# Kernel tuning notes

Measured on AMD Instinct MI355X. Metric: run time of the kernel, lower is better.

The kernel has to match this reference:

```python
import jax, jax.numpy as jnp
import numpy as np

N_QUBITS = 14
N_LAYERS = 6
BATCH = 512
DIM = 2 ** N_QUBITS

# Z expectation sign table: qubit 0 is the most-significant bit of the state index
_idx = np.arange(DIM)
_bits = np.stack([(_idx >> (N_QUBITS - 1 - q)) & 1 for q in range(N_QUBITS)])  # [n, DIM]
SIGNS = jnp.asarray(1.0 - 2.0 * _bits, dtype=jnp.float32)  # +1 for bit 0, -1 for bit 1


def _rx(theta):
    # 2x2 RX(theta) = [[cos(t/2), -i sin(t/2)], [-i sin(t/2), cos(t/2)]]
    c = jnp.cos(theta / 2).astype(jnp.complex64)
    s = ((-1j) * jnp.sin(theta / 2)).astype(jnp.complex64)
    return jnp.stack([jnp.stack([c, s]), jnp.stack([s, c])])


def _apply_1q(state, mat, q):
    # state: [B, 2^n] complex; apply 2x2 mat on qubit q
    left = 2 ** q
    right = 2 ** (N_QUBITS - 1 - q)
    s = state.reshape(-1, left, 2, right)
    s = jnp.einsum('ij,bljr->blir', mat, s)
    return s.reshape(-1, DIM)


def _apply_cnot(state, c, t):
    # CNOT(control=c, target=t): flip target bit where control bit is 1
    hi, lo = (c, t) if c < t else (t, c)
    A = 2 ** hi
    M = 2 ** (lo - hi - 1)
    R = 2 ** (N_QUBITS - 1 - lo)
    s = state.reshape(-1, A, 2, M, 2, R)
    if c < t:
        flipped = jnp.flip(s[:, :, 1:2, :, :, :], axis=4)
        s = jnp.concatenate([s[:, :, 0:1, :, :, :], flipped], axis=2)
    else:
        flipped = jnp.flip(s[:, :, :, :, 1:2, :], axis=2)
        s = jnp.concatenate([s[:, :, :, :, 0:1, :], flipped], axis=4)
    return s.reshape(-1, DIM)


def _forward(x, params):
    B = x.shape[0]
    # angle embedding in X basis: product state of RX(x_q)|0> per qubit
    half = 0.5 * x
    amps = jnp.stack([jnp.cos(half).astype(jnp.complex64),
                      ((-1j) * jnp.sin(half)).astype(jnp.complex64)], axis=-1)  # [B, n, 2]
    state = amps[:, 0]
    for q in range(1, N_QUBITS):
        state = (state[:, :, None] * amps[:, q][:, None, :]).reshape(B, -1)
    # basic_entangling ansatz: per-qubit RX then ring of CNOTs, per layer
    for layer in range(N_LAYERS):
        w = params[layer, 0]  # [n_qubits]
        for q in range(N_QUBITS):
            state = _apply_1q(state, _rx(w[q]), q)
        for q in range(N_QUBITS):
            state = _apply_cnot(state, q, (q + 1) % N_QUBITS)
    # <Z_q> expectation per qubit
    probs = state.real ** 2 + state.imag ** 2  # [B, DIM]
    return probs @ SIGNS.T  # [B, n_qubits]


def setup_inputs():
    key = jax.random.key(0)
    k1, k2 = jax.random.split(key)
    x = jax.random.normal(k1, (BATCH, N_QUBITS), dtype=jnp.float32)
    params = 2.0 * jnp.pi * jax.random.uniform(k2, (N_LAYERS, 1, N_QUBITS), dtype=jnp.float32)
    return {"x": x, "params": params}


def reference(x, params):
    return _forward(x, params)
```

## Files before the change

kernel.cpp:

```cpp
#include <hip/hip_runtime.h>
#include <math.h>


#define NQ 14
#define DIM 16384
#define NLAYERS 6
#define NGATES (NLAYERS * NQ)
#define BATCH 512
#define TB 1024
#define NREP 16
#define NSLICE 16
#define SLICE_B (BATCH / NSLICE)
#define B_PER_WAVE (SLICE_B * 64 / TB)

constexpr int cpopc(unsigned v) { int c = 0; while (v) { c += (int)(v & 1u); v >>= 1; } return c; }

constexpr unsigned cpext(unsigned v, unsigned m) {
    unsigned r = 0; int b = 0;
    for (int pos = 0; pos < 16; ++pos)
        if ((m >> pos) & 1u) { r |= ((v >> pos) & 1u) << b; ++b; }
    return r;
}

struct Tabs {
    unsigned short m[NGATES];
    unsigned short r[NQ];
    int p[NQ];
    int off[NQ + 1];
    unsigned char qb[NQ][NQ];
    int ng[NQ];
    unsigned short gmask[NQ][NGATES];
    unsigned char  gidx[NQ][NGATES];
};

constexpr Tabs gen_tabs() {
    Tabs T{};
    unsigned short C[NQ] = {}, R[NQ] = {};
    for (int q = 0; q < NQ; ++q) { C[q] = (unsigned short)(1u << (NQ - 1 - q)); R[q] = C[q]; }
    for (int l = 0; l < NLAYERS; ++l) {
        for (int q = 0; q < NQ; ++q) T.m[l * NQ + q] = C[q];
        for (int g = 0; g < NQ; ++g) {
            int t = (g + 1) % NQ;
            C[g] ^= C[t];
            R[t] ^= R[g];
        }
    }
    for (int q = 0; q < NQ; ++q) T.r[q] = R[q];
    for (int q = 0; q < NQ; ++q) {
        int cnt = 0;
        for (int pos = 0; pos < NQ; ++pos)
            if ((R[q] >> pos) & 1u) { T.qb[q][cnt] = (unsigned char)(NQ - 1 - pos); ++cnt; }
        T.p[q] = cnt;
    }
    T.off[0] = 0;
    for (int q = 0; q < NQ; ++q) T.off[q + 1] = T.off[q] + (1 << T.p[q]);
    for (int q = 0; q < NQ; ++q) {
        int n = 0;
        for (int g = 0; g < NGATES; ++g) {
            if (cpopc((unsigned)(T.m[g] & R[q])) & 1) {
                T.gmask[q][n] = T.m[g];
                T.gidx[q][n]  = (unsigned char)g;
                ++n;
            }
        }
        T.ng[q] = n;
    }
    return T;
}
constexpr Tabs TAB = gen_tabs();

constexpr int calc_maxp() { int m = 0; for (int q = 0; q < NQ; ++q) if (TAB.p[q] > m) m = TAB.p[q]; return m; }
constexpr int calc_minp() { int m = 99; for (int q = 0; q < NQ; ++q) if (TAB.p[q] < m) m = TAB.p[q]; return m; }
constexpr int MAXP  = calc_maxp();
constexpr int MINP  = calc_minp();
constexpr int TOTAL = TAB.off[NQ];
static_assert(MAXP <= 8, "u = t & (2^p-1) needs p <= 10; replicas sized for p <= 8");
static_assert(MINP >= 1, "r mask must be nonzero");

template<int Q, int I>
__device__ __forceinline__ void gates(const float2* __restrict__ w, int t,
                                      float (&Bx)[16], float (&By)[16])
{
    if constexpr (I < TAB.ng[Q]) {
        constexpr unsigned r  = TAB.r[Q];
        constexpr unsigned nr = (~r) & 0x3FFFu;
        constexpr int      p  = TAB.p[Q];
        constexpr unsigned mg = TAB.gmask[Q][I];
        constexpr unsigned Ag = cpext(mg, r);
        constexpr unsigned Bg = cpext(mg, nr);
        constexpr unsigned Mg = Ag | ((Bg & ((1u << (10 - p)) - 1u)) << p);
        constexpr unsigned Hg = (Bg >> (10 - p)) & 15u;
        const float2 wv = w[I];
        const float si = (__popc((unsigned)t & Mg) & 1) ? -wv.y : wv.y;
        const float c  = wv.x;
        const float nx = Bx[Hg] * c - By[Hg] * si;
        const float ny = Bx[Hg] * si + By[Hg] * c;
        Bx[Hg] = nx; By[Hg] = ny;
        gates<Q, I + 1>(w, t, Bx, By);
    }
}

template<int Q>
__device__ __forceinline__ void build_q(const float2* __restrict__ w,
                                        float* __restrict__ binC,
                                        float* __restrict__ binS, int t)
{
    constexpr int      p       = TAB.p[Q];
    constexpr unsigned lowmask = (1u << p) - 1u;

    float Bx[16], By[16];
    #pragma unroll
    for (int h = 0; h < 16; ++h) { Bx[h] = 1.0f; By[h] = 0.0f; }
    gates<Q, 0>(w, t, Bx, By);

    #pragma unroll
    for (int s = 1; s < 16; s <<= 1) {
        #pragma unroll
        for (int h = 0; h < 16; ++h) {
            if (!(h & s)) {
                const int h1 = h | s;
                const float p1 = Bx[h] * Bx[h1], p2 = By[h] * By[h1];
                const float p3 = Bx[h] * By[h1], p4 = By[h] * Bx[h1];
                Bx[h]  = p1 - p2;  By[h]  = p3 + p4;
                Bx[h1] = p1 + p2;  By[h1] = p4 - p3;
            }
        }
    }

    float fx = 0.0f, fy = 0.0f;
    #pragma unroll
    for (int h = 0; h < 16; ++h) { fx += Bx[h]; fy += By[h]; }

    const unsigned u   = (unsigned)t & lowmask;
    const int      rep = t >> 6;
    float* bc = binC + (rep << MAXP);
    float* bs = binS + (rep << MAXP);

    if constexpr (p >= 6) {
        bc[u] = fx;
        bs[u] = fy;
    } else {
        constexpr unsigned dm = 63u & ~lowmask;
        #pragma unroll
        for (int bb = p; bb < 6; ++bb) {
            fx += __shfl_xor(fx, 1 << bb, 64);
            fy += __shfl_xor(fy, 1 << bb, 64);
        }
        if (((unsigned)t & dm) == 0u) {
            bc[u] = fx;
            bs[u] = fy;
        }
    }
}

template<int Q>
__device__ __forceinline__ void run_q(const float2* __restrict__ w,
                                      float* __restrict__ binC,
                                      float* __restrict__ binS,
                                      float* __restrict__ tabC,
                                      float* __restrict__ tabS,
                                      const float* __restrict__ sxAll,
                                      float* __restrict__ out,
                                      int slice, int t)
{
    build_q<Q>(w, binC, binS, t);
    __syncthreads();

    constexpr int p  = TAB.p[Q];
    constexpr int nb = 1 << p;
    for (int i = t; i < nb; i += TB) {
        float sc = 0.0f, ss = 0.0f;
        #pragma unroll
        for (int rp = 0; rp < NREP; ++rp) {
            sc += binC[(rp << MAXP) + i];
            ss += binS[(rp << MAXP) + i];
        }
        tabC[i] = sc;
        tabS[i] = ss;
    }
    __syncthreads();

    const int wave = t >> 6;
    const int lane = t & 63;
    #pragma unroll
    for (int bb = 0; bb < B_PER_WAVE; ++bb) {
        const int bl = wave * B_PER_WAVE + bb;
        float acc = 0.0f;
        for (int u = lane; u < nb; u += 64) {
            float A = 0.0f;
            #pragma unroll
            for (int i = 0; i < p; ++i) {
                const float xv = sxAll[bl * NQ + TAB.qb[Q][i]];
                A += ((u >> i) & 1) ? xv : -xv;
            }
            float s, c;
            sincosf(A, &s, &c);
            acc += c * tabC[u] + s * tabS[u];
        }
        #pragma unroll
        for (int o = 32; o > 0; o >>= 1)
            acc += __shfl_down(acc, o, 64);
        if (lane == 0)
            out[(slice * SLICE_B + bl) * NQ + Q] = acc * (1.0f / (float)DIM);
    }
}

__global__ __launch_bounds__(TB, 4)
void fused_kernel(const float* __restrict__ x, const float* __restrict__ params,
                  float* __restrict__ out)
{
    __shared__ float2 w[NGATES];
    __shared__ float  binC[NREP << MAXP];
    __shared__ float  binS[NREP << MAXP];
    __shared__ float  tabC[1 << MAXP];
    __shared__ float  tabS[1 << MAXP];
    __shared__ float  sxAll[SLICE_B * NQ];

    const int q     = blockIdx.x % NQ;
    const int slice = blockIdx.x / NQ;
    const int t     = threadIdx.x;
    const int ng    = TAB.ng[q];

    if (t < ng) {
        const float th = params[(int)TAB.gidx[q][t]];
        float s, c; sincosf(th, &s, &c);
        w[t] = make_float2(c, s);
    }
    for (int i = t; i < (NREP << MAXP); i += TB) { binC[i] = 0.0f; binS[i] = 0.0f; }
    for (int i = t; i < SLICE_B * NQ; i += TB)   sxAll[i] = x[slice * (SLICE_B * NQ) + i];
    __syncthreads();

    switch (q) {
        case 0:  run_q<0 >(w, binC, binS, tabC, tabS, sxAll, out, slice, t); break;
        case 1:  run_q<1 >(w, binC, binS, tabC, tabS, sxAll, out, slice, t); break;
        case 2:  run_q<2 >(w, binC, binS, tabC, tabS, sxAll, out, slice, t); break;
        case 3:  run_q<3 >(w, binC, binS, tabC, tabS, sxAll, out, slice, t); break;
        case 4:  run_q<4 >(w, binC, binS, tabC, tabS, sxAll, out, slice, t); break;
        case 5:  run_q<5 >(w, binC, binS, tabC, tabS, sxAll, out, slice, t); break;
        case 6:  run_q<6 >(w, binC, binS, tabC, tabS, sxAll, out, slice, t); break;
        case 7:  run_q<7 >(w, binC, binS, tabC, tabS, sxAll, out, slice, t); break;
        case 8:  run_q<8 >(w, binC, binS, tabC, tabS, sxAll, out, slice, t); break;
        case 9:  run_q<9 >(w, binC, binS, tabC, tabS, sxAll, out, slice, t); break;
        case 10: run_q<10>(w, binC, binS, tabC, tabS, sxAll, out, slice, t); break;
        case 11: run_q<11>(w, binC, binS, tabC, tabS, sxAll, out, slice, t); break;
        case 12: run_q<12>(w, binC, binS, tabC, tabS, sxAll, out, slice, t); break;
        case 13: run_q<13>(w, binC, binS, tabC, tabS, sxAll, out, slice, t); break;
    }
}

extern "C" void kernel_launch(void* const* d_in, const int* in_sizes, int n_in,
                              void* d_out, int out_size, void* d_ws, size_t ws_size,
                              hipStream_t stream) {
    const float* x      = (const float*)d_in[0];
    const float* params = (const float*)d_in[1];
    float* out          = (float*)d_out;
    (void)d_ws; (void)ws_size;

    fused_kernel<<<NQ * NSLICE, TB, 0, stream>>>(x, params, out);
}
```

Before: 64.29 us.

## Prune final butterfly stages, hoist angle sums, use fast sincos and packed table

The last two butterfly stages are cut. Only the outputs that feed the final sum are computed, using a symmetry that lets the reduction become a doubled dot product. The evaluation loop now hoists the per-sample x values into registers, splits the angle sum into a lane-dependent part and a compile-time-unrolled high part, and uses __sincosf instead of sincosf. The cos/sin tables are packed into one float2 array for single LDS loads. The fast intrinsic sincos trades accuracy for speed, and the symmetry shortcut depends on the structure of the butterfly outputs.

After: 61.57 us. 1.04x faster.

```diff
diff --git a/kernel.cpp b/kernel.cpp
--- a/kernel.cpp
+++ b/kernel.cpp
@@ -114,7 +114,7 @@
     gates<Q, 0>(w, t, Bx, By);
 
     #pragma unroll
-    for (int s = 1; s < 16; s <<= 1) {
+    for (int s = 1; s < 4; s <<= 1) {
         #pragma unroll
         for (int h = 0; h < 16; ++h) {
             if (!(h & s)) {
@@ -126,10 +126,29 @@
             }
         }
     }
+    #pragma unroll
+    for (int h = 0; h < 4; ++h) {
+        const int h1 = h | 4;
+        const float p1 = Bx[h] * Bx[h1], p2 = By[h] * By[h1];
+        const float p3 = Bx[h] * By[h1], p4 = By[h] * Bx[h1];
+        Bx[h]  = p1 - p2;  By[h]  = p3 + p4;
+        Bx[h1] = p1 + p2;  By[h1] = p4 - p3;
+    }
+    #pragma unroll
+    for (int h = 8; h < 12; ++h) {
+        const int h1 = h | 4;
+        const float p1 = Bx[h] * Bx[h1], p2 = By[h] * By[h1];
+        Bx[h]  = p1 - p2;
+        Bx[h1] = p1 + p2;
+    }
 
     float fx = 0.0f, fy = 0.0f;
     #pragma unroll
-    for (int h = 0; h < 16; ++h) { fx += Bx[h]; fy += By[h]; }
+    for (int h = 0; h < 8; ++h) {
+        fx = fmaf(Bx[h | 8], Bx[h], fx);
+        fy = fmaf(Bx[h | 8], By[h], fy);
+    }
+    fx *= 2.0f; fy *= 2.0f;
 
     const unsigned u   = (unsigned)t & lowmask;
     const int      rep = t >> 6;
@@ -157,8 +176,7 @@
 __device__ __forceinline__ void run_q(const float2* __restrict__ w,
                                       float* __restrict__ binC,
                                       float* __restrict__ binS,
-                                      float* __restrict__ tabC,
-                                      float* __restrict__ tabS,
+                                      float2* __restrict__ tab2,
                                       const float* __restrict__ sxAll,
                                       float* __restrict__ out,
                                       int slice, int t)
@@ -175,8 +193,7 @@
             sc += binC[(rp << MAXP) + i];
             ss += binS[(rp << MAXP) + i];
         }
-        tabC[i] = sc;
-        tabS[i] = ss;
+        tab2[i] = make_float2(sc, ss);
     }
     __syncthreads();
 
@@ -185,18 +202,40 @@
     #pragma unroll
     for (int bb = 0; bb < B_PER_WAVE; ++bb) {
         const int bl = wave * B_PER_WAVE + bb;
+        const float* xr = sxAll + bl * NQ;
+        float xv[p];
+        #pragma unroll
+        for (int i = 0; i < p; ++i) xv[i] = xr[TAB.qb[Q][i]];
+
         float acc = 0.0f;
-        for (int u = lane; u < nb; u += 64) {
-            float A = 0.0f;
+        if constexpr (p >= 6) {
+            float A_low = 0.0f;
             #pragma unroll
-            for (int i = 0; i < p; ++i) {
-                const float xv = sxAll[bl * NQ + TAB.qb[Q][i]];
-                A += ((u >> i) & 1) ? xv : -xv;
-            }
-            float s, c;
-            sincosf(A, &s, &c);
-            acc += c * tabC[u] + s * tabS[u];
-        }
+            for (int i = 0; i < 6; ++i) A_low += ((lane >> i) & 1) ? xv[i] : -xv[i];
+            constexpr int HI = 1 << (p - 6);
+            #pragma unroll
+            for (int j = 0; j < HI; ++j) {
+                float A = A_low;
+                #pragma unroll
+                for (int i = 6; i < p; ++i) A += ((j >> (i - 6)) & 1) ? xv[i] : -xv[i];
+                const int u = lane + (j << 6);
+                float s, c;
+                __sincosf(A, &s, &c);
+                const float2 tv = tab2[u];
+                acc = fmaf(c, tv.x, fmaf(s, tv.y, acc));
+            }
+        } else {
+            if (lane < nb) {
+                float A = 0.0f;
+                #pragma unroll
+                for (int i = 0; i < p; ++i) A += ((lane >> i) & 1) ? xv[i] : -xv[i];
+                float s, c;
+                __sincosf(A, &s, &c);
+                const float2 tv = tab2[lane];
+                acc = fmaf(c, tv.x, fmaf(s, tv.y, acc));
+            }
+        }
+
         #pragma unroll
         for (int o = 32; o > 0; o >>= 1)
             acc += __shfl_down(acc, o, 64);
@@ -212,8 +251,7 @@
     __shared__ float2 w[NGATES];
     __shared__ float  binC[NREP << MAXP];
     __shared__ float  binS[NREP << MAXP];
-    __shared__ float  tabC[1 << MAXP];
-    __shared__ float  tabS[1 << MAXP];
+    __shared__ float2 tab2[1 << MAXP];
     __shared__ float  sxAll[SLICE_B * NQ];
 
     const int q     = blockIdx.x % NQ;
@@ -231,20 +269,20 @@
     __syncthreads();
 
     switch (q) {
-        case 0:  run_q<0 >(w, binC, binS, tabC, tabS, sxAll, out, slice, t); break;
-        case 1:  run_q<1 >(w, binC, binS, tabC, tabS, sxAll, out, slice, t); break;
-        case 2:  run_q<2 >(w, binC, binS, tabC, tabS, sxAll, out, slice, t); break;
-        case 3:  run_q<3 >(w, binC, binS, tabC, tabS, sxAll, out, slice, t); break;
-        case 4:  run_q<4 >(w, binC, binS, tabC, tabS, sxAll, out, slice, t); break;
-        case 5:  run_q<5 >(w, binC, binS, tabC, tabS, sxAll, out, slice, t); break;
-        case 6:  run_q<6 >(w, binC, binS, tabC, tabS, sxAll, out, slice, t); break;
-        case 7:  run_q<7 >(w, binC, binS, tabC, tabS, sxAll, out, slice, t); break;
-        case 8:  run_q<8 >(w, binC, binS, tabC, tabS, sxAll, out, slice, t); break;
-        case 9:  run_q<9 >(w, binC, binS, tabC, tabS, sxAll, out, slice, t); break;
-        case 10: run_q<10>(w, binC, binS, tabC, tabS, sxAll, out, slice, t); break;
-        case 11: run_q<11>(w, binC, binS, tabC, tabS, sxAll, out, slice, t); break;
-        case 12: run_q<12>(w, binC, binS, tabC, tabS, sxAll, out, slice, t); break;
-        case 13: run_q<13>(w, binC, binS, tabC, tabS, sxAll, out, slice, t); break;
+        case 0:  run_q<0 >(w, binC, binS, tab2, sxAll, out, slice, t); break;
+        case 1:  run_q<1 >(w, binC, binS, tab2, sxAll, out, slice, t); break;
+        case 2:  run_q<2 >(w, binC, binS, tab2, sxAll, out, slice, t); break;
+        case 3:  run_q<3 >(w, binC, binS, tab2, sxAll, out, slice, t); break;
+        case 4:  run_q<4 >(w, binC, binS, tab2, sxAll, out, slice, t); break;
+        case 5:  run_q<5 >(w, binC, binS, tab2, sxAll, out, slice, t); break;
+        case 6:  run_q<6 >(w, binC, binS, tab2, sxAll, out, slice, t); break;
+        case 7:  run_q<7 >(w, binC, binS, tab2, sxAll, out, slice, t); break;
+        case 8:  run_q<8 >(w, binC, binS, tab2, sxAll, out, slice, t); break;
+        case 9:  run_q<9 >(w, binC, binS, tab2, sxAll, out, slice, t); break;
+        case 10: run_q<10>(w, binC, binS, tab2, sxAll, out, slice, t); break;
+        case 11: run_q<11>(w, binC, binS, tab2, sxAll, out, slice, t); break;
+        case 12: run_q<12>(w, binC, binS, tab2, sxAll, out, slice, t); break;
+        case 13: run_q<13>(w, binC, binS, tab2, sxAll, out, slice, t); break;
     }
 }
 
```
